# Performance work log

Measured on AMD Instinct MI355X. Metric: run time of the kernel, lower is better.

Reference implementation:

```python
import jax, jax.numpy as jnp
import numpy as np

H = 4096      # number of hyperedges in the batch
N = 20000     # number of unique member nodes
FIN = 256     # in_features
FOUT = 128    # out_features
DEG = 32      # member nodes per hyperedge -> E = H*DEG incidence pairs


def setup_inputs() -> dict:
    key = jax.random.key(0)
    k1, k2, k3, k4 = jax.random.split(key, 4)
    xavier = 1.414 * np.sqrt(2.0 / (FIN + FOUT))  # gain=1.414 xavier scale
    hedge_embed = jax.random.normal(k1, (H, FIN), jnp.float32)
    node_embed = jax.random.normal(k2, (N, FIN), jnp.float32)
    Wq = jax.random.normal(k3, (FIN, FOUT), jnp.float32) * xavier
    # each hyperedge has exactly DEG member nodes (guarantees no empty softmax row)
    row_idx = jnp.repeat(jnp.arange(H, dtype=jnp.int64), DEG)
    col_idx = jax.random.randint(k4, (H * DEG,), 0, N, dtype=jnp.int64)
    return {"hedge_embed": hedge_embed, "node_embed": node_embed, "Wq": Wq,
            "row_idx": row_idx, "col_idx": col_idx}


def reference(hedge_embed, node_embed, Wq, row_idx, col_idx):
    # Faithful to NodeAttAggregator.compute:
    #   - queries AND keys both use query_weight (value_weight is unused in output)
    #   - mask filled with float64-min (overflows to -inf in fp32), member
    #     positions overwritten by scores, then row softmax
    #   - aggregation multiplies attention with the KEY projections
    q = hedge_embed @ Wq                                  # [H, FOUT]
    k = node_embed @ Wq                                   # [N, FOUT]
    scores = (q @ k.T) / jnp.sqrt(jnp.float32(FOUT))      # [H, N]
    member = jnp.zeros((H, N), dtype=bool).at[row_idx, col_idx].set(True)
    masked = jnp.where(member, scores, -jnp.inf)          # non-members -> -inf
    attn = jax.nn.softmax(masked, axis=1)                 # [H, N]
    out = (attn @ k).T                                    # [FOUT, H]
    return out
```

## Files before the change

kernel.cpp:

```cpp
#include <hip/hip_runtime.h>
#include <hip/hip_bf16.h>
#include <stdint.h>

#define H_EDGES 4096
#define N_NODES 20000
#define FIN 256
#define FOUT 128
#define DEG 32
#define ROWS_TOTAL 24096
#define G1_BLOCKS 377
#define A_F4_TOTAL 1542144
#define TOUCH_BLOCKS 1506

typedef float f32x4 __attribute__((ext_vector_type(4)));
typedef short s16x8 __attribute__((ext_vector_type(8)));
typedef unsigned short u16;

__device__ __forceinline__ u16 f2bf(float f) {
    return __builtin_bit_cast(u16, __float2bfloat16(f));
}
__device__ __forceinline__ float bf2f(u16 h) {
    unsigned u = ((unsigned)h) << 16;
    return __builtin_bit_cast(float, u);
}

__global__ __launch_bounds__(256)
void w0_prep(const float* __restrict__ Wq, const float* __restrict__ hedge,
             const float* __restrict__ node, u16* __restrict__ bt) {
    const int t = threadIdx.x;
    const int bid = blockIdx.x;
    if (bid < 16) {
        __shared__ u16 lt[32][72];
        const int kt = bid >> 2;
        const int ct = bid & 3;
        const int k0 = kt * 64, c0 = ct * 32;
        #pragma unroll
        for (int p = 0; p < 2; ++p) {
            const int r = p * 32 + (t >> 3);
            const int q = t & 7;
            f32x4 v = *(const f32x4*)(Wq + (size_t)(k0 + r) * FOUT + c0 + q * 4);
            #pragma unroll
            for (int j = 0; j < 4; ++j) lt[q * 4 + j][r] = f2bf(v[j]);
        }
        __syncthreads();
        const int cl = t >> 3;
        const int sl = t & 7;
        const int col = c0 + cl;
        const int s_glob = kt * 8 + sl;
        const int phys = s_glob ^ (col & 7);
        *(s16x8*)(bt + (size_t)(col * 32 + phys) * 8) = *(const s16x8*)&lt[cl][sl * 8];
    } else {
        const long base = (long)(bid - 16) * 1024 + t;
        float s = 0.f;
        #pragma unroll
        for (int j = 0; j < 4; ++j) {
            const long idx = base + j * 256;
            const f32x4* p = idx < 262144 ? (const f32x4*)hedge + idx
                                          : (const f32x4*)node + (idx - 262144);
            f32x4 v = *p;
            s += v[0] + v[1] + v[2] + v[3];
        }
        asm volatile("" :: "v"(s));
    }
}

__global__ __launch_bounds__(256)
void g1_gemm(const float* __restrict__ hedge, const float* __restrict__ node,
             const u16* __restrict__ bt, float* __restrict__ qf,
             u16* __restrict__ kb) {
    __shared__ u16 blds[FOUT * FIN];
    const int t = threadIdx.x;
    const int w = t >> 6, l = t & 63;
    const int lr = l & 15, lp = l >> 4;
    const long rb  = (long)blockIdx.x * 64 + w * 16;
    const long row = rb + lr;
    const long arow = row < ROWS_TOTAL ? row : ROWS_TOTAL - 1;
    const float* pa = arow < H_EDGES ? hedge + arow * FIN
                                     : node + (arow - H_EDGES) * FIN;

    f32x4 au[8], av[8];
    #pragma unroll
    for (int ks = 0; ks < 8; ++ks) {
        au[ks] = *(const f32x4*)(pa + ks * 32 + lp * 8);
        av[ks] = *(const f32x4*)(pa + ks * 32 + lp * 8 + 4);
    }

    {
        const s16x8* src = (const s16x8*)bt;
        s16x8* dst = (s16x8*)blds;
        #pragma unroll
        for (int j = 0; j < 16; ++j) { const int s = t + 256 * j; dst[s] = src[s]; }
    }
    __syncthreads();

    f32x4 acc[8];
    #pragma unroll
    for (int j = 0; j < 8; ++j) acc[j] = (f32x4){0.f, 0.f, 0.f, 0.f};

    #pragma unroll
    for (int ks = 0; ks < 8; ++ks) {
        s16x8 a;
        #pragma unroll
        for (int j = 0; j < 4; ++j) {
            a[j]     = (short)f2bf(au[ks][j]);
            a[j + 4] = (short)f2bf(av[ks][j]);
        }
        #pragma unroll
        for (int cf = 0; cf < 8; ++cf) {
            const int col = cf * 16 + lr;
            s16x8 b = *(const s16x8*)(blds +
                (size_t)(col * 32 + ((ks * 4 + lp) ^ (col & 7))) * 8);
            acc[cf] = __builtin_amdgcn_mfma_f32_16x16x32_bf16(a, b, acc[cf], 0, 0, 0);
        }
    }

    if (rb < H_EDGES) {
        #pragma unroll
        for (int i = 0; i < 4; ++i) {
            const long gr = rb + lp * 4 + i;
            #pragma unroll
            for (int cf = 0; cf < 8; ++cf)
                qf[gr * FOUT + cf * 16 + lr] = acc[cf][i];
        }
    } else {
        #pragma unroll
        for (int i = 0; i < 4; ++i) {
            const long gr = rb + lp * 4 + i;
            if (gr < ROWS_TOTAL) {
                #pragma unroll
                for (int cf = 0; cf < 8; ++cf)
                    kb[(gr - H_EDGES) * FOUT + cf * 16 + lr] = f2bf(acc[cf][i]);
            }
        }
    }
}

__global__ __launch_bounds__(256)
void g2_attn(const float* __restrict__ qf, const u16* __restrict__ kb,
             const int* __restrict__ col_idx, float* __restrict__ out) {
    __shared__ __align__(16) char smem[37888];
    const int t = threadIdx.x;
    const int w = t >> 6, l = t & 63;
    const int e = blockIdx.x * 4 + w;

    float (*tile)[4] = (float(*)[4])smem;
    char* base = smem + 2048 + w * 8960;
    u16*   kl  = (u16*)base;
    float* q_l = (float*)(base + 8192);
    float* w_l = q_l + 128;
    int*   c_l = (int*)(w_l + 32);

    if (l < DEG) c_l[l] = col_idx[(size_t)e * DEG + l];
    q_l[l]      = qf[(size_t)e * FOUT + l];
    q_l[l + 64] = qf[(size_t)e * FOUT + 64 + l];

    #pragma unroll
    for (int it = 0; it < 8; ++it) {
        const int s = l + 64 * it;
        const int m = s >> 4, sl = s & 15;
        const int phys = m * 16 + (sl & 8) + ((sl & 7) ^ (m & 7));
        *(s16x8*)(kl + (size_t)phys * 8) =
            *(const s16x8*)(kb + (size_t)c_l[m] * FOUT + sl * 8);
    }

    const int m = l >> 1, he = l & 1;
    float p = 0.f;
    #pragma unroll
    for (int j = 0; j < 8; ++j) {
        const int phys = m * 16 + he * 8 + (j ^ (m & 7));
        s16x8 kv = *(const s16x8*)(kl + (size_t)phys * 8);
        #pragma unroll
        for (int ee = 0; ee < 8; ++ee)
            p = fmaf(q_l[he * 64 + j * 8 + ee], bf2f((u16)kv[ee]), p);
    }
    p += __shfl_xor(p, 1);
    const float sc = p * 0.08838834764831845f;

    const int cm = c_l[m];
    bool valid = true;
    for (int j = 0; j < m; ++j)
        if (c_l[j] == cm) valid = false;
    const float sv = valid ? sc : -INFINITY;
    float mx = sv;
    #pragma unroll
    for (int d = 1; d < 64; d <<= 1) mx = fmaxf(mx, __shfl_xor(mx, d));
    const float ex = valid ? __expf(sv - mx) : 0.f;
    float sum = ex;
    #pragma unroll
    for (int d = 1; d < 64; d <<= 1) sum += __shfl_xor(sum, d);
    if (he == 0) w_l[m] = ex * 2.f / sum;

    const int sl0 = l >> 3, el = l & 7;
    float a0 = 0.f, a1 = 0.f;
    #pragma unroll
    for (int mm = 0; mm < DEG; ++mm) {
        const float wv = w_l[mm];
        const int p0 = mm * 16 + (sl0 ^ (mm & 7));
        a0 = fmaf(wv, bf2f(kl[(size_t)p0 * 8 + el]), a0);
        a1 = fmaf(wv, bf2f(kl[(size_t)(p0 + 8) * 8 + el]), a1);
    }

    tile[l][w]      = a0;
    tile[l + 64][w] = a1;
    __syncthreads();
    if (t < FOUT) {
        f32x4 v = *(const f32x4*)tile[t];
        *(f32x4*)(out + (size_t)t * H_EDGES + blockIdx.x * 4) = v;
    }
}

extern "C" void kernel_launch(void* const* d_in, const int* in_sizes, int n_in,
                              void* d_out, int out_size, void* d_ws, size_t ws_size,
                              hipStream_t stream) {
    const float* hedge   = (const float*)d_in[0];
    const float* node    = (const float*)d_in[1];
    const float* Wq      = (const float*)d_in[2];
    const int*   col_idx = (const int*)d_in[4];
    float* out = (float*)d_out;

    char* ws = (char*)d_ws;
    float* qf = (float*)ws;
    u16*   kb = (u16*)(ws + (size_t)H_EDGES * FOUT * 4);
    u16*   bt = (u16*)(ws + (size_t)H_EDGES * FOUT * 4
                          + (size_t)N_NODES * FOUT * 2);

    w0_prep<<<16 + TOUCH_BLOCKS, 256, 0, stream>>>(Wq, hedge, node, bt);
    g1_gemm<<<G1_BLOCKS, 256, 0, stream>>>(hedge, node, bt, qf, kb);
    g2_attn<<<H_EDGES / 4, 256, 0, stream>>>(qf, kb, col_idx, out);
}
```

Measured before the change: 29.60 us.

## Keep gathered key rows in registers and drop LDS staging in attention kernel

The attention kernel now holds each hyperedge's 32 gathered bf16 key rows in registers. Dot products, the duplicate check and the weighted sum use wave shuffles instead of a large per-wave LDS staging buffer, which cuts shared memory from about 37 KB to under 3 KB and adds a launch-bounds occupancy hint. The aim is to remove the LDS round trip and raise occupancy. It also drops the max subtraction before the exponential, which assumes the scores stay small enough not to overflow.

```diff
diff --git a/kernel.cpp b/kernel.cpp
--- a/kernel.cpp
+++ b/kernel.cpp
@@ -9,7 +9,6 @@
 #define DEG 32
 #define ROWS_TOTAL 24096
 #define G1_BLOCKS 377
-#define A_F4_TOTAL 1542144
 #define TOUCH_BLOCKS 1506
 
 typedef float f32x4 __attribute__((ext_vector_type(4)));
@@ -135,73 +134,91 @@
     }
 }
 
-__global__ __launch_bounds__(256)
+__global__ __launch_bounds__(256, 4)
 void g2_attn(const float* __restrict__ qf, const u16* __restrict__ kb,
              const int* __restrict__ col_idx, float* __restrict__ out) {
-    __shared__ __align__(16) char smem[37888];
+    __shared__ __align__(16) char smem[2688];
+    float (*tile)[4] = (float(*)[4])smem;
     const int t = threadIdx.x;
     const int w = t >> 6, l = t & 63;
+    const int g = l >> 4, sl = l & 15;
     const int e = blockIdx.x * 4 + w;
-
-    float (*tile)[4] = (float(*)[4])smem;
-    char* base = smem + 2048 + w * 8960;
-    u16*   kl  = (u16*)base;
-    float* q_l = (float*)(base + 8192);
-    float* w_l = q_l + 128;
-    int*   c_l = (int*)(w_l + 32);
-
-    if (l < DEG) c_l[l] = col_idx[(size_t)e * DEG + l];
-    q_l[l]      = qf[(size_t)e * FOUT + l];
-    q_l[l + 64] = qf[(size_t)e * FOUT + 64 + l];
-
+    float* s_l = (float*)(smem + 2048) + w * 32;
+
+    const int creg = col_idx[(size_t)e * DEG + (l & 31)];
+
+    const float* qp = qf + (size_t)e * FOUT + sl * 8;
+    const f32x4 qa = *(const f32x4*)qp;
+    const f32x4 qb = *(const f32x4*)(qp + 4);
+
+    s16x8 kreg[8];
     #pragma unroll
     for (int it = 0; it < 8; ++it) {
-        const int s = l + 64 * it;
-        const int m = s >> 4, sl = s & 15;
-        const int phys = m * 16 + (sl & 8) + ((sl & 7) ^ (m & 7));
-        *(s16x8*)(kl + (size_t)phys * 8) =
-            *(const s16x8*)(kb + (size_t)c_l[m] * FOUT + sl * 8);
-    }
-
-    const int m = l >> 1, he = l & 1;
-    float p = 0.f;
-    #pragma unroll
-    for (int j = 0; j < 8; ++j) {
-        const int phys = m * 16 + he * 8 + (j ^ (m & 7));
-        s16x8 kv = *(const s16x8*)(kl + (size_t)phys * 8);
-        #pragma unroll
-        for (int ee = 0; ee < 8; ++ee)
-            p = fmaf(q_l[he * 64 + j * 8 + ee], bf2f((u16)kv[ee]), p);
-    }
-    p += __shfl_xor(p, 1);
-    const float sc = p * 0.08838834764831845f;
-
-    const int cm = c_l[m];
-    bool valid = true;
-    for (int j = 0; j < m; ++j)
-        if (c_l[j] == cm) valid = false;
-    const float sv = valid ? sc : -INFINITY;
-    float mx = sv;
-    #pragma unroll
-    for (int d = 1; d < 64; d <<= 1) mx = fmaxf(mx, __shfl_xor(mx, d));
-    const float ex = valid ? __expf(sv - mx) : 0.f;
+        const int cm = __shfl(creg, it * 4 + g);
+        kreg[it] = *(const s16x8*)(kb + (size_t)cm * FOUT + sl * 8);
+    }
+
+    float p[8];
+    #pragma unroll
+    for (int it = 0; it < 8; ++it) {
+        float s = 0.f;
+        #pragma unroll
+        for (int j = 0; j < 4; ++j) {
+            s = fmaf(qa[j], bf2f((u16)kreg[it][j]), s);
+            s = fmaf(qb[j], bf2f((u16)kreg[it][j + 4]), s);
+        }
+        s += __shfl_xor(s, 1);
+        s += __shfl_xor(s, 2);
+        s += __shfl_xor(s, 4);
+        s += __shfl_xor(s, 8);
+        p[it] = s * 0.08838834764831845f;
+    }
+
+    #pragma unroll
+    for (int it = 0; it < 8; ++it)
+        if (sl == it) s_l[it * 4 + g] = p[it];
+
+    const int m2 = l >> 1, he = l & 1;
+    const int cm2 = __shfl(creg, m2);
+    int dup = 0;
+    #pragma unroll
+    for (int jj = 0; jj < 16; ++jj) {
+        const int j = he * 16 + jj;
+        const int cj = __shfl(creg, j);
+        dup |= (j < m2 && cj == cm2) ? 1 : 0;
+    }
+    dup |= __shfl_xor(dup, 1);
+    const float sv = s_l[m2];
+    const float ex = dup ? 0.f : __expf(sv);
     float sum = ex;
     #pragma unroll
     for (int d = 1; d < 64; d <<= 1) sum += __shfl_xor(sum, d);
-    if (he == 0) w_l[m] = ex * 2.f / sum;
-
-    const int sl0 = l >> 3, el = l & 7;
-    float a0 = 0.f, a1 = 0.f;
-    #pragma unroll
-    for (int mm = 0; mm < DEG; ++mm) {
-        const float wv = w_l[mm];
-        const int p0 = mm * 16 + (sl0 ^ (mm & 7));
-        a0 = fmaf(wv, bf2f(kl[(size_t)p0 * 8 + el]), a0);
-        a1 = fmaf(wv, bf2f(kl[(size_t)(p0 + 8) * 8 + el]), a1);
-    }
-
-    tile[l][w]      = a0;
-    tile[l + 64][w] = a1;
+    const float wgt = ex * 2.f / sum;
+
+    f32x4 aa = (f32x4){0.f, 0.f, 0.f, 0.f};
+    f32x4 ab = (f32x4){0.f, 0.f, 0.f, 0.f};
+    #pragma unroll
+    for (int it = 0; it < 8; ++it) {
+        const float wm = __shfl(wgt, (it * 4 + g) * 2);
+        #pragma unroll
+        for (int j = 0; j < 4; ++j) {
+            aa[j] = fmaf(wm, bf2f((u16)kreg[it][j]), aa[j]);
+            ab[j] = fmaf(wm, bf2f((u16)kreg[it][j + 4]), ab[j]);
+        }
+    }
+    #pragma unroll
+    for (int j = 0; j < 4; ++j) {
+        aa[j] += __shfl_xor(aa[j], 16); aa[j] += __shfl_xor(aa[j], 32);
+        ab[j] += __shfl_xor(ab[j], 16); ab[j] += __shfl_xor(ab[j], 32);
+    }
+
+    if (g == 0) {
+        #pragma unroll
+        for (int j = 0; j < 4; ++j) {
+            tile[sl * 8 + j][w]     = aa[j];
+            tile[sl * 8 + 4 + j][w] = ab[j];
+        }
+    }
     __syncthreads();
     if (t < FOUT) {
         f32x4 v = *(const f32x4*)tile[t];
```

Measured after the change: 30.78 us. 4.0% more time.
